# Performance work log

Hardware: AMD Instinct MI355X
Metric: run time of the kernel (lower is better)

## Reference

```python
import jax, jax.numpy as jnp
import numpy as np

B, S = 8, 2048
D_IN, D_STATE, D_OUT = 1024, 1024, 1024
H = 16
DH = D_STATE // H  # 64
N_LAYERS = 24
STD = 0.02
EPS = 1e-6


def setup_inputs() -> dict:
    key = jax.random.key(0)
    k = jax.random.split(key, 4)
    x = jax.random.normal(k[0], (B, S, D_IN), dtype=jnp.float32)
    # input_projection: Linear(D_IN, 4*D_STATE, bias=False), std=0.02
    w_in = jax.random.normal(k[1], (D_IN, 4 * D_STATE), dtype=jnp.float32) * STD
    # state_weight: [3*H, DH, DH] recurrence matrices (candidate, forget, reset)
    state_weight = jax.random.normal(k[2], (3 * H, DH, DH), dtype=jnp.float32) * STD
    # rmsnorm weight over state_size
    norm_weight = jnp.ones((D_STATE,), dtype=jnp.float32)
    # output_projection: Linear(D_STATE, D_OUT, bias=False), std scaled by sqrt(2*num_layers)
    w_out = jax.random.normal(k[3], (D_STATE, D_OUT), dtype=jnp.float32) * (STD / np.sqrt(2 * N_LAYERS))
    return {"x": x, "w_in": w_in, "state_weight": state_weight,
            "norm_weight": norm_weight, "w_out": w_out}


def _rmsnorm(x, w):
    var = jnp.mean(jnp.square(x), axis=-1, keepdims=True)
    return x * jax.lax.rsqrt(var + EPS) * w


def reference(x, w_in, state_weight, norm_weight, w_out):
    # input projection -> [B, S, 4*D_STATE]
    proj = jnp.einsum('bsi,io->bso', x, w_in)
    xg, g = jnp.split(proj, [3 * D_STATE], axis=-1)
    xi, xf, xr = jnp.split(xg, 3, axis=-1)
    # per-head views [B, S, H, DH]
    xi = xi.reshape(B, S, H, DH)
    xf = xf.reshape(B, S, H, DH)
    xr = xr.reshape(B, S, H, DH)
    W, Wf, Wr = jnp.split(state_weight, 3, axis=0)  # each [H, DH, DH]

    # scan over time: carry h [B, H, DH]
    def step(h, inp):
        xi_t, xf_t, xr_t = inp  # each [B, H, DH]
        r = jax.nn.sigmoid(xr_t + jnp.einsum('bhd,hde->bhe', h, Wr))
        f = jax.nn.sigmoid(xf_t + jnp.einsum('bhd,hde->bhe', h, Wf))
        c = jnp.tanh(xi_t + jnp.einsum('bhd,hde->bhe', r * h, W))
        h_new = f * h + (1.0 - f) * c
        return h_new, h_new

    h0 = jnp.zeros((B, H, DH), dtype=x.dtype)
    xs = (jnp.swapaxes(xi, 0, 1), jnp.swapaxes(xf, 0, 1), jnp.swapaxes(xr, 0, 1))
    _, hs = jax.lax.scan(step, h0, xs)  # hs: [S, B, H, DH]
    h_seq = jnp.swapaxes(hs, 0, 1).reshape(B, S, D_STATE)

    # gated output: h * silu(g), rmsnorm, output projection
    y = h_seq * jax.nn.silu(g)
    y = _rmsnorm(y, norm_weight)
    return jnp.einsum('bsd,do->bso', y, w_out)
```

## Files before the change

### kernel.cpp

```cpp
#include <hip/hip_runtime.h>
#include <hip/hip_bf16.h>
#include <math.h>

typedef __hip_bfloat16 bf16;

#define B_      8
#define S_      2048
#define DIN     1024
#define DSTATE  1024
#define H_      16
#define DH_     64
#define PROJ4   4096

#define BARRIER_LGKM() asm volatile("s_waitcnt lgkmcnt(0)\n\ts_barrier" ::: "memory")

__device__ __forceinline__ unsigned short f2bf(float f) {
    unsigned int x = __float_as_uint(f);
    x += 0x7FFFu + ((x >> 16) & 1u);
    return (unsigned short)(x >> 16);
}

__device__ __forceinline__ float4 load4(const float* p) { return *(const float4*)p; }
__device__ __forceinline__ float4 load4(const bf16* p) {
    uint2 u = *(const uint2*)p;
    float4 r;
    r.x = __uint_as_float((u.x & 0xFFFFu) << 16);
    r.y = __uint_as_float(u.x & 0xFFFF0000u);
    r.z = __uint_as_float((u.y & 0xFFFFu) << 16);
    r.w = __uint_as_float(u.y & 0xFFFF0000u);
    return r;
}
__device__ __forceinline__ void store4(float* p, float4 v) { *(float4*)p = v; }
__device__ __forceinline__ void store4(bf16* p, float4 v) {
    uint2 u;
    u.x = (unsigned int)f2bf(v.x) | ((unsigned int)f2bf(v.y) << 16);
    u.y = (unsigned int)f2bf(v.z) | ((unsigned int)f2bf(v.w) << 16);
    *(uint2*)p = u;
}

typedef __attribute__((ext_vector_type(8))) short bf16x8;
typedef __attribute__((ext_vector_type(4))) float f32x4;
typedef __attribute__((ext_vector_type(2))) float f32x2;
typedef __attribute__((ext_vector_type(4))) short short4v;

template <typename TA>
__device__ __forceinline__ void load_a4(const TA* p, float out[4]);
template <>
__device__ __forceinline__ void load_a4<float>(const float* p, float out[4]) {
    float4 v = *(const float4*)p;
    out[0] = v.x; out[1] = v.y; out[2] = v.z; out[3] = v.w;
}
template <>
__device__ __forceinline__ void load_a4<bf16>(const bf16* p, float out[4]) {
    float4 v = load4(p);
    out[0] = v.x; out[1] = v.y; out[2] = v.z; out[3] = v.w;
}

template <typename TA, typename TC>
__global__ __launch_bounds__(256) void gemm_mfma(const TA* __restrict__ A,
                                                 const float* __restrict__ Bm,
                                                 TC* __restrict__ C,
                                                 int M, int N, int K, int lda) {
    __shared__ short As[128][40];
    __shared__ short Bs[128][40];

    const int tid = threadIdx.x;
    const int m0 = blockIdx.y * 128;
    const int n0 = blockIdx.x * 128;

    const int saM = tid >> 1;
    const int saK = (tid & 1) * 16;
    const int sbK = tid >> 3;
    const int sbN = (tid & 7) * 16;

    const int wid = tid >> 6;
    const int wx = wid & 1, wy = wid >> 1;
    const int lane = tid & 63;
    const int c16 = lane & 15;
    const int quad = lane >> 4;

    const TA* Aptr = A + (size_t)(m0 + saM) * lda + saK;
    const float* Bptr = Bm + (size_t)sbK * N + n0 + sbN;

    f32x4 acc[4][4];
    #pragma unroll
    for (int i = 0; i < 4; ++i)
        #pragma unroll
        for (int j = 0; j < 4; ++j) acc[i][j] = (f32x4){0.f, 0.f, 0.f, 0.f};

    float ra[4][4];
    float rb[4][4];
    #pragma unroll
    for (int i = 0; i < 4; ++i) load_a4<TA>(Aptr + i * 4, ra[i]);
    #pragma unroll
    for (int i = 0; i < 4; ++i) {
        float4 v = load4(Bptr + i * 4);
        rb[i][0] = v.x; rb[i][1] = v.y; rb[i][2] = v.z; rb[i][3] = v.w;
    }

    for (int k0 = 0; k0 < K; k0 += 32) {
        __syncthreads();
        #pragma unroll
        for (int i = 0; i < 4; ++i) {
            short4v pk = { (short)f2bf(ra[i][0]), (short)f2bf(ra[i][1]),
                           (short)f2bf(ra[i][2]), (short)f2bf(ra[i][3]) };
            *(short4v*)&As[saM][saK + i * 4] = pk;
        }
        #pragma unroll
        for (int i = 0; i < 4; ++i)
            #pragma unroll
            for (int j = 0; j < 4; ++j)
                Bs[sbN + i * 4 + j][sbK] = (short)f2bf(rb[i][j]);
        __syncthreads();

        if (k0 + 32 < K) {
            #pragma unroll
            for (int i = 0; i < 4; ++i) load_a4<TA>(Aptr + k0 + 32 + i * 4, ra[i]);
            #pragma unroll
            for (int i = 0; i < 4; ++i) {
                float4 v = load4(Bptr + (size_t)(k0 + 32) * N + i * 4);
                rb[i][0] = v.x; rb[i][1] = v.y; rb[i][2] = v.z; rb[i][3] = v.w;
            }
        }

        bf16x8 af[4], bfr[4];
        #pragma unroll
        for (int mt = 0; mt < 4; ++mt)
            af[mt] = *(const bf16x8*)&As[wy * 64 + mt * 16 + c16][quad * 8];
        #pragma unroll
        for (int nt = 0; nt < 4; ++nt)
            bfr[nt] = *(const bf16x8*)&Bs[wx * 64 + nt * 16 + c16][quad * 8];

        #pragma unroll
        for (int mt = 0; mt < 4; ++mt)
            #pragma unroll
            for (int nt = 0; nt < 4; ++nt)
                acc[mt][nt] = __builtin_amdgcn_mfma_f32_16x16x32_bf16(
                    af[mt], bfr[nt], acc[mt][nt], 0, 0, 0);
    }

    #pragma unroll
    for (int mt = 0; mt < 4; ++mt) {
        #pragma unroll
        for (int r = 0; r < 4; ++r) {
            int row = m0 + wy * 64 + mt * 16 + quad * 4 + r;
            TC* cp = C + (size_t)row * N + n0 + wx * 64;
            #pragma unroll
            for (int nt = 0; nt < 4; ++nt)
                cp[nt * 16 + c16] = (TC)acc[mt][nt][r];
        }
    }
}

__device__ __forceinline__ float lane_bcast(float v, int lane) {
    return __int_as_float(__builtin_amdgcn_readlane(__float_as_int(v), lane));
}

#define RPT16(M) M(0) M(1) M(2) M(3) M(4) M(5) M(6) M(7) \
                 M(8) M(9) M(10) M(11) M(12) M(13) M(14) M(15)

__global__ __launch_bounds__(256, 1)
__attribute__((amdgpu_waves_per_eu(1, 1)))
void recur_kernel(bf16* __restrict__ proj, const float* __restrict__ sw) {
    const int tid = threadIdx.x;
    const int e = tid & 63;
    const int w = __builtin_amdgcn_readfirstlane(tid >> 6);
    const int d0 = w << 4;
    const int bh = blockIdx.x;
    const int b = bh >> 4;
    const int h = bh & 15;

    __shared__ float2 part_rf[4][64];
    __shared__ float  part_c[4][64];

    const float* Wc_p = sw + (size_t)h * 4096 + (size_t)d0 * 64 + e;
    const float* Wf_p = Wc_p + (size_t)16 * 4096;
    const float* Wr_p = Wc_p + (size_t)32 * 4096;

    #define DECLW(i) float wc##i, wf##i, wr##i;
    RPT16(DECLW)
    #undef DECLW
    #define LOADW(i) wc##i = Wc_p[(i) * 64]; \
                     wf##i = Wf_p[(i) * 64]; \
                     wr##i = Wr_p[(i) * 64];
    RPT16(LOADW)
    #undef LOADW
    #define PINW(i) asm volatile("" : "+v"(wc##i), "+v"(wf##i), "+v"(wr##i));
    RPT16(PINW)
    #undef PINW

    bf16* xi_p = proj + (size_t)b * S_ * PROJ4 + h * 64 + e;

    f32x4 rxi, rxf, rxr;
    #define PRELOAD(U) { const bf16* p = xi_p + (size_t)(U) * PROJ4; \
        rxi[U] = __bfloat162float(p[0]); \
        rxf[U] = __bfloat162float(p[1024]); \
        rxr[U] = __bfloat162float(p[2048]); }
    PRELOAD(0) PRELOAD(1) PRELOAD(2) PRELOAD(3)
    #undef PRELOAD

    float hreg = 0.0f;

    const bf16* ld = xi_p + (size_t)4 * PROJ4;
    bf16*       st = xi_p;

    #define P1T(i, A) { float hb = lane_bcast(hreg, d0 + (i)); \
        aR##A = fmaf(hb, wr##i, aR##A); \
        aF##A = fmaf(hb, wf##i, aF##A); }
    #define P2T(i, A) { float qb = lane_bcast(rh, d0 + (i)); \
        aC##A = fmaf(qb, wc##i, aC##A); }

    #define STEP(U, REFILL) { \
        float xi0 = rxi[U], xf0 = rxf[U], xr0 = rxr[U]; \
        if (REFILL) { \
            const bf16* p = ld + (size_t)(U) * PROJ4; \
            rxi[U] = __bfloat162float(p[0]); \
            rxf[U] = __bfloat162float(p[1024]); \
            rxr[U] = __bfloat162float(p[2048]); \
        } \
        float aR0 = 0.f, aR1 = 0.f, aF0 = 0.f, aF1 = 0.f; \
        P1T(0,0)  P1T(1,1)  P1T(2,0)  P1T(3,1) \
        P1T(4,0)  P1T(5,1)  P1T(6,0)  P1T(7,1) \
        P1T(8,0)  P1T(9,1)  P1T(10,0) P1T(11,1) \
        P1T(12,0) P1T(13,1) P1T(14,0) P1T(15,1) \
        part_rf[w][e] = make_float2(aR0 + aR1, aF0 + aF1); \
        BARRIER_LGKM(); \
        float2 p0 = part_rf[0][e], p1 = part_rf[1][e]; \
        float2 p2 = part_rf[2][e], p3 = part_rf[3][e]; \
        float sr = xr0 + (p0.x + p1.x) + (p2.x + p3.x); \
        float sf = xf0 + (p0.y + p1.y) + (p2.y + p3.y); \
        float r = 1.f / (1.f + __expf(-sr)); \
        float f = 1.f / (1.f + __expf(-sf)); \
        float rh = r * hreg; \
        float aC0 = 0.f, aC1 = 0.f; \
        P2T(0,0)  P2T(1,1)  P2T(2,0)  P2T(3,1) \
        P2T(4,0)  P2T(5,1)  P2T(6,0)  P2T(7,1) \
        P2T(8,0)  P2T(9,1)  P2T(10,0) P2T(11,1) \
        P2T(12,0) P2T(13,1) P2T(14,0) P2T(15,1) \
        part_c[w][e] = aC0 + aC1; \
        BARRIER_LGKM(); \
        float sc = xi0 + (part_c[0][e] + part_c[1][e]) \
                       + (part_c[2][e] + part_c[3][e]); \
        sc = fminf(fmaxf(sc, -15.f), 15.f); \
        float ex = __expf(-2.f * sc); \
        float cc = (1.f - ex) / (1.f + ex); \
        hreg = f * hreg + (1.f - f) * cc; \
        if (w == (U)) st[(size_t)(U) * PROJ4] = __float2bfloat16(hreg); \
    }

    for (int t0 = 0; t0 < S_ - 4; t0 += 4) {
        STEP(0, 1) STEP(1, 1) STEP(2, 1) STEP(3, 1)
        ld += (size_t)4 * PROJ4;
        st += (size_t)4 * PROJ4;
    }
    STEP(0, 0) STEP(1, 0) STEP(2, 0) STEP(3, 0)

    #undef STEP
    #undef P1T
    #undef P2T
}

__global__ __launch_bounds__(256) void gate_norm_kernel(bf16* __restrict__ proj,
                                                        const float* __restrict__ nw) {
    const int row = blockIdx.x;
    const int tid = threadIdx.x;
    __shared__ float red[4];

    bf16* hp = proj + (size_t)row * PROJ4;
    const bf16* gp = hp + 3 * DSTATE;

    float4 hv = load4(hp + tid * 4);
    float4 gv = load4(gp + tid * 4);

    float v0 = hv.x * (gv.x / (1.f + __expf(-gv.x)));
    float v1 = hv.y * (gv.y / (1.f + __expf(-gv.y)));
    float v2 = hv.z * (gv.z / (1.f + __expf(-gv.z)));
    float v3 = hv.w * (gv.w / (1.f + __expf(-gv.w)));

    float ss = v0 * v0 + v1 * v1 + v2 * v2 + v3 * v3;
    #pragma unroll
    for (int mask = 32; mask >= 1; mask >>= 1)
        ss += __shfl_xor(ss, mask, 64);

    const int wid = tid >> 6;
    if ((tid & 63) == 0) red[wid] = ss;
    __syncthreads();
    float tot = red[0] + red[1] + red[2] + red[3];
    float scale = rsqrtf(tot * (1.0f / (float)DSTATE) + 1e-6f);

    float4 nv = *(const float4*)(nw + tid * 4);
    float4 y;
    y.x = v0 * scale * nv.x;
    y.y = v1 * scale * nv.y;
    y.z = v2 * scale * nv.z;
    y.w = v3 * scale * nv.w;
    store4(hp + tid * 4, y);
}

extern "C" void kernel_launch(void* const* d_in, const int* in_sizes, int n_in,
                              void* d_out, int out_size, void* d_ws, size_t ws_size,
                              hipStream_t stream) {
    const float* x     = (const float*)d_in[0];
    const float* w_in  = (const float*)d_in[1];
    const float* sw    = (const float*)d_in[2];
    const float* nw    = (const float*)d_in[3];
    const float* w_out = (const float*)d_in[4];
    float* out = (float*)d_out;

    bf16* proj = (bf16*)d_ws;

    dim3 g1(PROJ4 / 128, (B_ * S_) / 128);
    gemm_mfma<float, bf16><<<g1, 256, 0, stream>>>(x, w_in, proj,
                                                   B_ * S_, PROJ4, DIN, DIN);

    recur_kernel<<<128, 256, 0, stream>>>(proj, sw);

    gate_norm_kernel<<<B_ * S_, 256, 0, stream>>>(proj, nw);

    dim3 g2(DSTATE / 128, (B_ * S_) / 128);
    gemm_mfma<bf16, float><<<g2, 256, 0, stream>>>(proj, w_out, out,
                                                   B_ * S_, DSTATE, DSTATE, PROJ4);
}
```

Before: 1.732 ms.

## Fuse projection GEMM, recurrence, norm and output GEMM into one persistent pipelined kernel

Replaces four separate launches with a single persistent kernel. 128 blocks run the recurrence per (batch, head) over 128-step time chunks, and the remaining blocks pull input-projection tiles and later norm+output-projection tiles from atomic work queues. Global counters let the recurrence start a chunk as soon as its projection tiles exist, and let the output GEMM start as soon as all heads finish a chunk, so the GEMMs overlap with the serial scan. This relies on all 256 blocks being co-resident and on spin-wait flags, which risks deadlock or contention. It also gives the recurrence blocks a normal occupancy hint instead of the dedicated one-wave-per-EU setting.

```diff
diff --git a/kernel.cpp b/kernel.cpp
--- a/kernel.cpp
+++ b/kernel.cpp
@@ -11,8 +11,21 @@
 #define H_      16
 #define DH_     64
 #define PROJ4   4096
+#define NT1     4096
+#define NU2     128
 
 #define BARRIER_LGKM() asm volatile("s_waitcnt lgkmcnt(0)\n\ts_barrier" ::: "memory")
+
+__device__ int g_q1;
+__device__ int g_q2;
+__device__ int g_rc[128];
+__device__ int g_rd[128];
+
+__global__ void zero_flags() {
+    int i = threadIdx.x;
+    if (i == 0) { g_q1 = 0; g_q2 = 0; }
+    if (i < 128) { g_rc[i] = 0; g_rd[i] = 0; }
+}
 
 __device__ __forceinline__ unsigned short f2bf(float f) {
     unsigned int x = __float_as_uint(f);
@@ -40,7 +53,6 @@
 
 typedef __attribute__((ext_vector_type(8))) short bf16x8;
 typedef __attribute__((ext_vector_type(4))) float f32x4;
-typedef __attribute__((ext_vector_type(2))) float f32x2;
 typedef __attribute__((ext_vector_type(4))) short short4v;
 
 template <typename TA>
@@ -57,22 +69,14 @@
 }
 
 template <typename TA, typename TC>
-__global__ __launch_bounds__(256) void gemm_mfma(const TA* __restrict__ A,
-                                                 const float* __restrict__ Bm,
-                                                 TC* __restrict__ C,
-                                                 int M, int N, int K, int lda) {
-    __shared__ short As[128][40];
-    __shared__ short Bs[128][40];
-
+__device__ void gemm_tile(const TA* __restrict__ A, const float* __restrict__ Bm,
+                          TC* __restrict__ C, int N, int K, int lda,
+                          int m0, int n0, short* As, short* Bs) {
     const int tid = threadIdx.x;
-    const int m0 = blockIdx.y * 128;
-    const int n0 = blockIdx.x * 128;
-
     const int saM = tid >> 1;
     const int saK = (tid & 1) * 16;
     const int sbK = tid >> 3;
     const int sbN = (tid & 7) * 16;
-
     const int wid = tid >> 6;
     const int wx = wid & 1, wy = wid >> 1;
     const int lane = tid & 63;
@@ -104,13 +108,13 @@
         for (int i = 0; i < 4; ++i) {
             short4v pk = { (short)f2bf(ra[i][0]), (short)f2bf(ra[i][1]),
                            (short)f2bf(ra[i][2]), (short)f2bf(ra[i][3]) };
-            *(short4v*)&As[saM][saK + i * 4] = pk;
+            *(short4v*)&As[saM * 40 + saK + i * 4] = pk;
         }
         #pragma unroll
         for (int i = 0; i < 4; ++i)
             #pragma unroll
             for (int j = 0; j < 4; ++j)
-                Bs[sbN + i * 4 + j][sbK] = (short)f2bf(rb[i][j]);
+                Bs[(sbN + i * 4 + j) * 40 + sbK] = (short)f2bf(rb[i][j]);
         __syncthreads();
 
         if (k0 + 32 < K) {
@@ -126,10 +130,10 @@
         bf16x8 af[4], bfr[4];
         #pragma unroll
         for (int mt = 0; mt < 4; ++mt)
-            af[mt] = *(const bf16x8*)&As[wy * 64 + mt * 16 + c16][quad * 8];
+            af[mt] = *(const bf16x8*)&As[(wy * 64 + mt * 16 + c16) * 40 + quad * 8];
         #pragma unroll
         for (int nt = 0; nt < 4; ++nt)
-            bfr[nt] = *(const bf16x8*)&Bs[wx * 64 + nt * 16 + c16][quad * 8];
+            bfr[nt] = *(const bf16x8*)&Bs[(wx * 64 + nt * 16 + c16) * 40 + quad * 8];
 
         #pragma unroll
         for (int mt = 0; mt < 4; ++mt)
@@ -152,120 +156,10 @@
     }
 }
 
-__device__ __forceinline__ float lane_bcast(float v, int lane) {
-    return __int_as_float(__builtin_amdgcn_readlane(__float_as_int(v), lane));
-}
-
-#define RPT16(M) M(0) M(1) M(2) M(3) M(4) M(5) M(6) M(7) \
-                 M(8) M(9) M(10) M(11) M(12) M(13) M(14) M(15)
-
-__global__ __launch_bounds__(256, 1)
-__attribute__((amdgpu_waves_per_eu(1, 1)))
-void recur_kernel(bf16* __restrict__ proj, const float* __restrict__ sw) {
+__device__ __forceinline__ void gn_row(bf16* __restrict__ proj,
+                                       const float* __restrict__ nw,
+                                       int row, float* red) {
     const int tid = threadIdx.x;
-    const int e = tid & 63;
-    const int w = __builtin_amdgcn_readfirstlane(tid >> 6);
-    const int d0 = w << 4;
-    const int bh = blockIdx.x;
-    const int b = bh >> 4;
-    const int h = bh & 15;
-
-    __shared__ float2 part_rf[4][64];
-    __shared__ float  part_c[4][64];
-
-    const float* Wc_p = sw + (size_t)h * 4096 + (size_t)d0 * 64 + e;
-    const float* Wf_p = Wc_p + (size_t)16 * 4096;
-    const float* Wr_p = Wc_p + (size_t)32 * 4096;
-
-    #define DECLW(i) float wc##i, wf##i, wr##i;
-    RPT16(DECLW)
-    #undef DECLW
-    #define LOADW(i) wc##i = Wc_p[(i) * 64]; \
-                     wf##i = Wf_p[(i) * 64]; \
-                     wr##i = Wr_p[(i) * 64];
-    RPT16(LOADW)
-    #undef LOADW
-    #define PINW(i) asm volatile("" : "+v"(wc##i), "+v"(wf##i), "+v"(wr##i));
-    RPT16(PINW)
-    #undef PINW
-
-    bf16* xi_p = proj + (size_t)b * S_ * PROJ4 + h * 64 + e;
-
-    f32x4 rxi, rxf, rxr;
-    #define PRELOAD(U) { const bf16* p = xi_p + (size_t)(U) * PROJ4; \
-        rxi[U] = __bfloat162float(p[0]); \
-        rxf[U] = __bfloat162float(p[1024]); \
-        rxr[U] = __bfloat162float(p[2048]); }
-    PRELOAD(0) PRELOAD(1) PRELOAD(2) PRELOAD(3)
-    #undef PRELOAD
-
-    float hreg = 0.0f;
-
-    const bf16* ld = xi_p + (size_t)4 * PROJ4;
-    bf16*       st = xi_p;
-
-    #define P1T(i, A) { float hb = lane_bcast(hreg, d0 + (i)); \
-        aR##A = fmaf(hb, wr##i, aR##A); \
-        aF##A = fmaf(hb, wf##i, aF##A); }
-    #define P2T(i, A) { float qb = lane_bcast(rh, d0 + (i)); \
-        aC##A = fmaf(qb, wc##i, aC##A); }
-
-    #define STEP(U, REFILL) { \
-        float xi0 = rxi[U], xf0 = rxf[U], xr0 = rxr[U]; \
-        if (REFILL) { \
-            const bf16* p = ld + (size_t)(U) * PROJ4; \
-            rxi[U] = __bfloat162float(p[0]); \
-            rxf[U] = __bfloat162float(p[1024]); \
-            rxr[U] = __bfloat162float(p[2048]); \
-        } \
-        float aR0 = 0.f, aR1 = 0.f, aF0 = 0.f, aF1 = 0.f; \
-        P1T(0,0)  P1T(1,1)  P1T(2,0)  P1T(3,1) \
-        P1T(4,0)  P1T(5,1)  P1T(6,0)  P1T(7,1) \
-        P1T(8,0)  P1T(9,1)  P1T(10,0) P1T(11,1) \
-        P1T(12,0) P1T(13,1) P1T(14,0) P1T(15,1) \
-        part_rf[w][e] = make_float2(aR0 + aR1, aF0 + aF1); \
-        BARRIER_LGKM(); \
-        float2 p0 = part_rf[0][e], p1 = part_rf[1][e]; \
-        float2 p2 = part_rf[2][e], p3 = part_rf[3][e]; \
-        float sr = xr0 + (p0.x + p1.x) + (p2.x + p3.x); \
-        float sf = xf0 + (p0.y + p1.y) + (p2.y + p3.y); \
-        float r = 1.f / (1.f + __expf(-sr)); \
-        float f = 1.f / (1.f + __expf(-sf)); \
-        float rh = r * hreg; \
-        float aC0 = 0.f, aC1 = 0.f; \
-        P2T(0,0)  P2T(1,1)  P2T(2,0)  P2T(3,1) \
-        P2T(4,0)  P2T(5,1)  P2T(6,0)  P2T(7,1) \
-        P2T(8,0)  P2T(9,1)  P2T(10,0) P2T(11,1) \
-        P2T(12,0) P2T(13,1) P2T(14,0) P2T(15,1) \
-        part_c[w][e] = aC0 + aC1; \
-        BARRIER_LGKM(); \
-        float sc = xi0 + (part_c[0][e] + part_c[1][e]) \
-                       + (part_c[2][e] + part_c[3][e]); \
-        sc = fminf(fmaxf(sc, -15.f), 15.f); \
-        float ex = __expf(-2.f * sc); \
-        float cc = (1.f - ex) / (1.f + ex); \
-        hreg = f * hreg + (1.f - f) * cc; \
-        if (w == (U)) st[(size_t)(U) * PROJ4] = __float2bfloat16(hreg); \
-    }
-
-    for (int t0 = 0; t0 < S_ - 4; t0 += 4) {
-        STEP(0, 1) STEP(1, 1) STEP(2, 1) STEP(3, 1)
-        ld += (size_t)4 * PROJ4;
-        st += (size_t)4 * PROJ4;
-    }
-    STEP(0, 0) STEP(1, 0) STEP(2, 0) STEP(3, 0)
-
-    #undef STEP
-    #undef P1T
-    #undef P2T
-}
-
-__global__ __launch_bounds__(256) void gate_norm_kernel(bf16* __restrict__ proj,
-                                                        const float* __restrict__ nw) {
-    const int row = blockIdx.x;
-    const int tid = threadIdx.x;
-    __shared__ float red[4];
-
     bf16* hp = proj + (size_t)row * PROJ4;
     const bf16* gp = hp + 3 * DSTATE;
 
@@ -282,8 +176,7 @@
     for (int mask = 32; mask >= 1; mask >>= 1)
         ss += __shfl_xor(ss, mask, 64);
 
-    const int wid = tid >> 6;
-    if ((tid & 63) == 0) red[wid] = ss;
+    if ((tid & 63) == 0) red[tid >> 6] = ss;
     __syncthreads();
     float tot = red[0] + red[1] + red[2] + red[3];
     float scale = rsqrtf(tot * (1.0f / (float)DSTATE) + 1e-6f);
@@ -295,6 +188,188 @@
     y.z = v2 * scale * nv.z;
     y.w = v3 * scale * nv.w;
     store4(hp + tid * 4, y);
+    __syncthreads();
+}
+
+__device__ __forceinline__ float lane_bcast(float v, int lane) {
+    return __int_as_float(__builtin_amdgcn_readlane(__float_as_int(v), lane));
+}
+
+#define RPT16(M) M(0) M(1) M(2) M(3) M(4) M(5) M(6) M(7) \
+                 M(8) M(9) M(10) M(11) M(12) M(13) M(14) M(15)
+
+__global__ __launch_bounds__(256) void fused_kernel(
+        const float* __restrict__ x, const float* __restrict__ w_in,
+        const float* __restrict__ sw, const float* __restrict__ nw,
+        const float* __restrict__ w_out, bf16* __restrict__ proj,
+        float* __restrict__ out) {
+    __shared__ __align__(16) char smem[57344];
+    const int tid = threadIdx.x;
+    const int bid = blockIdx.x;
+
+    if (bid < 128) {
+        float2* prf = (float2*)smem;
+        float*  pc  = (float*)(smem + 2048);
+
+        const int e = tid & 63;
+        const int w = __builtin_amdgcn_readfirstlane(tid >> 6);
+        const int d0 = w << 4;
+        const int b = bid >> 4;
+        const int h = bid & 15;
+
+        const float* Wc_p = sw + (size_t)h * 4096 + (size_t)d0 * 64 + e;
+        const float* Wf_p = Wc_p + (size_t)16 * 4096;
+        const float* Wr_p = Wc_p + (size_t)32 * 4096;
+
+        #define DECLW(i) float wc##i, wf##i, wr##i;
+        RPT16(DECLW)
+        #undef DECLW
+        #define LOADW(i) wc##i = Wc_p[(i) * 64]; \
+                         wf##i = Wf_p[(i) * 64]; \
+                         wr##i = Wr_p[(i) * 64];
+        RPT16(LOADW)
+        #undef LOADW
+        #define PINW(i) asm volatile("" : "+v"(wc##i), "+v"(wf##i), "+v"(wr##i));
+        RPT16(PINW)
+        #undef PINW
+
+        bf16* xi_p = proj + (size_t)b * S_ * PROJ4 + h * 64 + e;
+        float hreg = 0.0f;
+
+        #define P1T(i, A) { float hb = lane_bcast(hreg, d0 + (i)); \
+            aR##A = fmaf(hb, wr##i, aR##A); \
+            aF##A = fmaf(hb, wf##i, aF##A); }
+        #define P2T(i, A) { float qb = lane_bcast(rh, d0 + (i)); \
+            aC##A = fmaf(qb, wc##i, aC##A); }
+
+        #define STEP(U, REFILL) { \
+            float xi0 = rxi[U], xf0 = rxf[U], xr0 = rxr[U]; \
+            if (REFILL) { \
+                const bf16* p = ld + (size_t)(U) * PROJ4; \
+                rxi[U] = __bfloat162float(p[0]); \
+                rxf[U] = __bfloat162float(p[1024]); \
+                rxr[U] = __bfloat162float(p[2048]); \
+            } \
+            float aR0 = 0.f, aR1 = 0.f, aF0 = 0.f, aF1 = 0.f; \
+            P1T(0,0)  P1T(1,1)  P1T(2,0)  P1T(3,1) \
+            P1T(4,0)  P1T(5,1)  P1T(6,0)  P1T(7,1) \
+            P1T(8,0)  P1T(9,1)  P1T(10,0) P1T(11,1) \
+            P1T(12,0) P1T(13,1) P1T(14,0) P1T(15,1) \
+            prf[w * 64 + e] = make_float2(aR0 + aR1, aF0 + aF1); \
+            BARRIER_LGKM(); \
+            float2 p0 = prf[0 * 64 + e], p1 = prf[1 * 64 + e]; \
+            float2 p2 = prf[2 * 64 + e], p3 = prf[3 * 64 + e]; \
+            float sr = xr0 + (p0.x + p1.x) + (p2.x + p3.x); \
+            float sf = xf0 + (p0.y + p1.y) + (p2.y + p3.y); \
+            float r = 1.f / (1.f + __expf(-sr)); \
+            float f = 1.f / (1.f + __expf(-sf)); \
+            float rh = r * hreg; \
+            float aC0 = 0.f, aC1 = 0.f; \
+            P2T(0,0)  P2T(1,1)  P2T(2,0)  P2T(3,1) \
+            P2T(4,0)  P2T(5,1)  P2T(6,0)  P2T(7,1) \
+            P2T(8,0)  P2T(9,1)  P2T(10,0) P2T(11,1) \
+            P2T(12,0) P2T(13,1) P2T(14,0) P2T(15,1) \
+            pc[w * 64 + e] = aC0 + aC1; \
+            BARRIER_LGKM(); \
+            float sc = xi0 + (pc[0 * 64 + e] + pc[1 * 64 + e]) \
+                           + (pc[2 * 64 + e] + pc[3 * 64 + e]); \
+            sc = fminf(fmaxf(sc, -15.f), 15.f); \
+            float ex = __expf(-2.f * sc); \
+            float cc = (1.f - ex) / (1.f + ex); \
+            hreg = f * hreg + (1.f - f) * cc; \
+            if (w == (U)) st[(size_t)(U) * PROJ4] = __float2bfloat16(hreg); \
+        }
+
+        for (int tc = 0; tc < 16; ++tc) {
+            const int mIdx = b * 16 + tc;
+            if (tid == 0) {
+                while (__hip_atomic_load(&g_rc[mIdx], __ATOMIC_RELAXED,
+                                         __HIP_MEMORY_SCOPE_AGENT) < 32)
+                    __builtin_amdgcn_s_sleep(8);
+            }
+            __syncthreads();
+            __threadfence();
+
+            bf16* xrow = xi_p + (size_t)(tc * 128) * PROJ4;
+            f32x4 rxi, rxf, rxr;
+            #define PRELOAD(U) { const bf16* p = xrow + (size_t)(U) * PROJ4; \
+                rxi[U] = __bfloat162float(p[0]); \
+                rxf[U] = __bfloat162float(p[1024]); \
+                rxr[U] = __bfloat162float(p[2048]); }
+            PRELOAD(0) PRELOAD(1) PRELOAD(2) PRELOAD(3)
+            #undef PRELOAD
+
+            const bf16* ld = xrow + (size_t)4 * PROJ4;
+            bf16*       st = xrow;
+
+            for (int t0 = 0; t0 < 124; t0 += 4) {
+                STEP(0, 1) STEP(1, 1) STEP(2, 1) STEP(3, 1)
+                ld += (size_t)4 * PROJ4;
+                st += (size_t)4 * PROJ4;
+            }
+            STEP(0, 0) STEP(1, 0) STEP(2, 0) STEP(3, 0)
+
+            __syncthreads();
+            if (tid == 0) {
+                __threadfence();
+                atomicAdd(&g_rd[mIdx], 1);
+            }
+        }
+        #undef STEP
+        #undef P1T
+        #undef P2T
+    } else {
+        short* As   = (short*)smem;
+        short* Bs   = (short*)(smem + 10240);
+        int*  taskp = (int*)(smem + 20480);
+        float* red  = (float*)(smem + 20484);
+
+        for (;;) {
+            __syncthreads();
+            if (tid == 0) *taskp = atomicAdd(&g_q1, 1);
+            __syncthreads();
+            int id = *taskp;
+            if (id >= NT1) break;
+            int tc = id >> 8;
+            int rem = id & 255;
+            int bb = rem >> 5;
+            int n = rem & 31;
+            int mIdx = bb * 16 + tc;
+            gemm_tile<float, bf16>(x, w_in, proj, PROJ4, DIN, DIN,
+                                   mIdx * 128, n * 128, As, Bs);
+            __syncthreads();
+            if (tid == 0) {
+                __threadfence();
+                atomicAdd(&g_rc[mIdx], 1);
+            }
+        }
+
+        for (;;) {
+            __syncthreads();
+            if (tid == 0) *taskp = atomicAdd(&g_q2, 1);
+            __syncthreads();
+            int id = *taskp;
+            if (id >= NU2) break;
+            int tc = id >> 3;
+            int bb = id & 7;
+            int mIdx = bb * 16 + tc;
+            if (tid == 0) {
+                while (__hip_atomic_load(&g_rd[mIdx], __ATOMIC_RELAXED,
+                                         __HIP_MEMORY_SCOPE_AGENT) < 16)
+                    __builtin_amdgcn_s_sleep(8);
+            }
+            __syncthreads();
+            __threadfence();
+
+            int rbase = mIdx * 128;
+            for (int r = 0; r < 128; ++r) gn_row(proj, nw, rbase + r, red);
+            __syncthreads();
+
+            for (int nt = 0; nt < 8; ++nt)
+                gemm_tile<bf16, float>(proj, w_out, out, DSTATE, DSTATE, PROJ4,
+                                       rbase, nt * 128, As, Bs);
+        }
+    }
 }
 
 extern "C" void kernel_launch(void* const* d_in, const int* in_sizes, int n_in,
@@ -309,15 +384,6 @@
 
     bf16* proj = (bf16*)d_ws;
 
-    dim3 g1(PROJ4 / 128, (B_ * S_) / 128);
-    gemm_mfma<float, bf16><<<g1, 256, 0, stream>>>(x, w_in, proj,
-                                                   B_ * S_, PROJ4, DIN, DIN);
-
-    recur_kernel<<<128, 256, 0, stream>>>(proj, sw);
-
-    gate_norm_kernel<<<B_ * S_, 256, 0, stream>>>(proj, nw);
-
-    dim3 g2(DSTATE / 128, (B_ * S_) / 128);
-    gemm_mfma<bf16, float><<<g2, 256, 0, stream>>>(proj, w_out, out,
-                                                   B_ * S_, DSTATE, DSTATE, PROJ4);
-}
+    zero_flags<<<1, 128, 0, stream>>>();
+    fused_kernel<<<256, 256, 0, stream>>>(x, w_in, sw, nw, w_out, proj, out);
+}
```

After: 2.216 ms. 27.9% more time.
